# Optimization experiments

Hardware: AMD Instinct MI355X
Metric: run time of the kernel (lower is better)

Reference implementation:

```python
import jax, jax.numpy as jnp
import numpy as np

N = 256          # num agents
HID = 128        # hidden_dim
ACT = 5          # action_dim
NH = 4           # num_heads
D = HID + 16     # concat_hidden_dim = 144
E = D * NH       # mha embed dim = 576
HD = D           # per-head dim = E // NH = 144
OBS_RX, OBS_RY = 4, 2   # obs_r from fov_size=(9,5)
GRID = 40


def setup_inputs() -> dict:
    key = jax.random.key(0)
    ks = jax.random.split(key, 24)
    g = lambda k, shape, s: (jax.random.normal(k, shape, dtype=jnp.float32) * s)
    inp = {
        "hidden_state_n": g(ks[0], (N, HID), 1.0),
        "action_n": g(ks[1], (N, HID), 1.0),
        "state_n": jax.random.randint(ks[2], (N, 2), 0, GRID, dtype=jnp.int32),
        # obs encoder
        "W_enc": g(ks[3], (HID, 16), HID ** -0.5), "b_enc": jnp.zeros((16,), jnp.float32),
        # MHABlock outer projections
        "Wq": g(ks[4], (D, E), D ** -0.5), "bq": jnp.zeros((E,), jnp.float32),
        "Wk": g(ks[5], (D, E), D ** -0.5), "bk": jnp.zeros((E,), jnp.float32),
        "Wv": g(ks[6], (D, E), D ** -0.5), "bv": jnp.zeros((E,), jnp.float32),
        # nn.MultiheadAttention internal in/out projections
        "Wiq": g(ks[7], (E, E), E ** -0.5), "biq": jnp.zeros((E,), jnp.float32),
        "Wik": g(ks[8], (E, E), E ** -0.5), "bik": jnp.zeros((E,), jnp.float32),
        "Wiv": g(ks[9], (E, E), E ** -0.5), "biv": jnp.zeros((E,), jnp.float32),
        "Wo_proj": g(ks[10], (E, E), E ** -0.5), "bo_proj": jnp.zeros((E,), jnp.float32),
        "W_O": g(ks[11], (E, D), E ** -0.5),  # no bias
        # dueling decoders
        "W_val": g(ks[12], (D, 1), D ** -0.5), "b_val": jnp.zeros((1,), jnp.float32),
        "W_adv": g(ks[13], (D, ACT), D ** -0.5), "b_adv": jnp.zeros((ACT,), jnp.float32),
    }
    return inp


def reference(hidden_state_n, action_n, W_enc, b_enc, Wq, bq, Wk, bk, Wv, bv,
              Wiq, biq, Wik, bik, Wiv, biv, Wo_proj, bo_proj, W_O,
              W_val, b_val, W_adv, b_adv, state_n):
    n = hidden_state_n.shape[0]
    # observed_agents[i] = {j > i : |x_i-x_j|<=rx and |y_i-y_j|<=ry}
    pos = state_n.astype(jnp.int32)
    dx = jnp.abs(pos[:, None, 0] - pos[None, :, 0])
    dy = jnp.abs(pos[:, None, 1] - pos[None, :, 1])
    upper = jnp.arange(n)[None, :] > jnp.arange(n)[:, None]
    mask = (dx <= OBS_RX) & (dy <= OBS_RY) & upper            # [N,N], mask[i,j]: j observed by i

    # per-neighbor feature c_j = concat(obs_encoder(h_j), a_j)  -> [N, D]
    obs = hidden_state_n @ W_enc + b_enc                       # [N,16]
    C = jnp.concatenate([obs, action_n], axis=-1)              # [N,D]

    # MHABlock: outer Q/K/V projections then nn.MultiheadAttention
    q = (C @ Wq + bq) @ Wiq + biq                              # [N,E]
    k = (C @ Wk + bk) @ Wik + bik
    v = (C @ Wv + bv) @ Wiv + biv
    q2 = q.reshape(n, NH, HD)
    k2 = k.reshape(n, NH, HD)
    v2 = v.reshape(n, NH, HD)

    scale = 1.0 / np.sqrt(HD).astype(np.float32)
    S = jnp.einsum("jhd,khd->hjk", q2, k2) * scale             # [H,N,N] shared across agents

    pair = (mask[:, None, :, None] & mask[:, None, None, :])   # [N,1,Nq,Nk]
    logits = jnp.where(pair, S[None, :, :, :], -1e9)           # [N,H,N,N]
    m = jnp.max(logits, axis=-1, keepdims=True)
    p = jnp.exp(logits - m) * pair.astype(logits.dtype)
    attn = p / jnp.maximum(p.sum(axis=-1, keepdims=True), 1e-9)

    ctx = jnp.einsum("ihjk,khd->ijhd", attn, v2).reshape(n, n, E)  # [N,Nq,E]
    out = (ctx @ Wo_proj + bo_proj) @ W_O                          # [N,Nq,D]

    # sum over the (masked) neighbor/query axis -> per-agent h_i
    h = jnp.sum(out * mask[:, :, None].astype(out.dtype), axis=1)  # [N,D]

    V = h @ W_val + b_val                                          # [N,1]
    A = h @ W_adv + b_adv                                          # [N,ACT]
    Q = V + A - jnp.mean(A, axis=-1, keepdims=True)                # dueling Q
    return Q
```

## Files before the change

kernel.cpp:

```cpp
#include <hip/hip_runtime.h>

#define NAG 256
#define HID 128
#define ACT 5
#define NH 4
#define DD 144
#define EE 576
#define HDIM 144
#define CMAX 32

#define STEP4(acc, a) do { \
    acc.x += (a).x*wc0.x + (a).y*wc1.x + (a).z*wc2.x + (a).w*wc3.x; \
    acc.y += (a).x*wc0.y + (a).y*wc1.y + (a).z*wc2.y + (a).w*wc3.y; \
    acc.z += (a).x*wc0.z + (a).y*wc1.z + (a).z*wc2.z + (a).w*wc3.z; \
    acc.w += (a).x*wc0.w + (a).y*wc1.w + (a).z*wc2.w + (a).w*wc3.w; } while (0)

__device__ __forceinline__ void gemm8x64_sk(
    const float* __restrict__ A,
    const float* __restrict__ Wt,
    const float* __restrict__ bv,
    const float* __restrict__ rs,
    const float* __restrict__ rb,
    float* __restrict__ outp,
    int K, int lda, int ldw, int ldo, int nvalid,
    int tid, float* __restrict__ sm)
{
    const int lsa = K + 4;
    const int KF4 = K >> 2;
    for (int idx = tid; idx < 8 * KF4; idx += 256) {
        int r = idx / KF4, f = idx - r * KF4;
        *((float4*)&sm[r * lsa + f * 4]) =
            *(const float4*)(A + (size_t)r * lda + f * 4);
    }
    __syncthreads();
    const int wave = tid >> 6, lane = tid & 63;
    const int cg = lane & 15, rg = lane >> 4;
    const int co = cg * 4;
    const bool cok = (co + 4 <= nvalid);
    const int Kq = K >> 2;
    const int kbase = wave * Kq;
    const float* Wp = Wt + (size_t)kbase * ldw + (cok ? co : 0);
    float4 acc0 = {0.f, 0.f, 0.f, 0.f}, acc1 = {0.f, 0.f, 0.f, 0.f};
    float4 wc0, wc1, wc2, wc3;
    wc0 = *(const float4*)(Wp);
    wc1 = *(const float4*)(Wp + (size_t)ldw);
    wc2 = *(const float4*)(Wp + 2 * (size_t)ldw);
    wc3 = *(const float4*)(Wp + 3 * (size_t)ldw);
    const float* Asr = sm + (rg * 2) * lsa + kbase;
    const int NG = Kq >> 2;
    for (int g = 0; g < NG; ++g) {
        float4 nx0, nx1, nx2, nx3;
        if (g + 1 < NG) {
            const float* Wn = Wp + (size_t)(4 * (g + 1)) * ldw;
            nx0 = *(const float4*)(Wn);
            nx1 = *(const float4*)(Wn + (size_t)ldw);
            nx2 = *(const float4*)(Wn + 2 * (size_t)ldw);
            nx3 = *(const float4*)(Wn + 3 * (size_t)ldw);
        }
        float4 a0 = *((const float4*)(Asr + g * 4));
        float4 a1 = *((const float4*)(Asr + lsa + g * 4));
        STEP4(acc0, a0);
        STEP4(acc1, a1);
        wc0 = nx0; wc1 = nx1; wc2 = nx2; wc3 = nx3;
    }
    __syncthreads();
    float* red = sm;
    *((float4*)&red[wave * 512 + (rg * 2 + 0) * 64 + co]) = acc0;
    *((float4*)&red[wave * 512 + (rg * 2 + 1) * 64 + co]) = acc1;
    __syncthreads();
    #pragma unroll
    for (int qq = 0; qq < 2; ++qq) {
        int idx = tid + qq * 256;
        int r = idx >> 6, cl = idx & 63;
        if (cl < nvalid) {
            float s = red[idx] + red[512 + idx] + red[1024 + idx] + red[1536 + idx];
            float add = bv ? bv[cl] : 0.f;
            if (rs) add += rs[r] * rb[cl];
            outp[(size_t)r * ldo + cl] = s + add;
        }
    }
}

__global__ __launch_bounds__(256) void k_enc(
    const float* __restrict__ hidden, const float* __restrict__ action,
    const float* __restrict__ W_enc, const float* __restrict__ b_enc,
    float* __restrict__ C)
{
    __shared__ float Hs[8 * 132];
    __shared__ float We[2048];
    const int mb = blockIdx.x, tid = threadIdx.x;
    {
        int r = tid >> 5, kq = tid & 31;
        *((float4*)&Hs[r * 132 + kq * 4]) =
            *(const float4*)(hidden + (size_t)(mb * 8 + r) * HID + kq * 4);
        float4 a4 = *(const float4*)(action + (size_t)(mb * 8 + r) * HID + kq * 4);
        *((float4*)(C + (size_t)(mb * 8 + r) * DD + 16 + kq * 4)) = a4;
        *((float4*)&We[tid * 4])        = *(const float4*)(W_enc + tid * 4);
        *((float4*)&We[1024 + tid * 4]) = *(const float4*)(W_enc + 1024 + tid * 4);
    }
    __syncthreads();
    if (tid < 128) {
        int r = tid >> 4, o = tid & 15;
        float acc = 0.f;
        #pragma unroll 8
        for (int d = 0; d < HID; ++d) acc += Hs[r * 132 + d] * We[d * 16 + o];
        C[(size_t)(mb * 8 + r) * DD + o] = acc + b_enc[o];
    }
}

__global__ __launch_bounds__(256) void k_t3(
    const float* __restrict__ C,
    const float* __restrict__ Wq, const float* __restrict__ bq,
    const float* __restrict__ Wk, const float* __restrict__ bk,
    const float* __restrict__ Wv, const float* __restrict__ bv,
    float* __restrict__ Tq, float* __restrict__ Tk, float* __restrict__ Tv)
{
    __shared__ float sm[2048];
    const int z = blockIdx.z;
    const float* W = (z == 0) ? Wq : (z == 1) ? Wk : Wv;
    const float* b = (z == 0) ? bq : (z == 1) ? bk : bv;
    float*       T = (z == 0) ? Tq : (z == 1) ? Tk : Tv;
    const int rbase = blockIdx.x * 8, cb = blockIdx.y * 64;
    gemm8x64_sk(C + (size_t)rbase * DD, W + cb, b + cb, nullptr, nullptr,
                T + (size_t)rbase * EE + cb, DD, DD, EE, EE, 64,
                threadIdx.x, sm);
}

__global__ __launch_bounds__(256) void k_qkv3(
    const float* __restrict__ Tq, const float* __restrict__ Tk, const float* __restrict__ Tv,
    const float* __restrict__ Wiq, const float* __restrict__ biq,
    const float* __restrict__ Wik, const float* __restrict__ bik,
    const float* __restrict__ Wiv, const float* __restrict__ biv,
    float* __restrict__ q, float* __restrict__ kb, float* __restrict__ v)
{
    __shared__ float sm[8 * 580];
    const int z = blockIdx.z;
    const float* A = (z == 0) ? Tq  : (z == 1) ? Tk  : Tv;
    const float* W = (z == 0) ? Wiq : (z == 1) ? Wik : Wiv;
    const float* b = (z == 0) ? biq : (z == 1) ? bik : biv;
    float*       o = (z == 0) ? q   : (z == 1) ? kb  : v;
    const int rbase = blockIdx.x * 8, cb = blockIdx.y * 64;
    gemm8x64_sk(A + (size_t)rbase * EE, W + cb, b + cb, nullptr, nullptr,
                o + (size_t)rbase * EE + cb, EE, EE, EE, EE, 64,
                threadIdx.x, sm);
}

#define DOT4(a, b) ((a).x*(b).x + (a).y*(b).y + (a).z*(b).z + (a).w*(b).w)

__global__ __launch_bounds__(64) void k_score(
    const float* __restrict__ q, const float* __restrict__ kmat,
    float* __restrict__ S)
{
    __shared__ float Aq[8 * 148];
    __shared__ float Bk[64 * 148];
    const int tid = threadIdx.x;
    const int jb = blockIdx.x * 8, kbb = blockIdx.y * 64, h = blockIdx.z;
    const float* Ap = q    + (size_t)jb  * EE + h * HDIM;
    const float* Bp = kmat + (size_t)kbb * EE + h * HDIM;
    for (int idx = tid; idx < 8 * 36; idx += 64) {
        int r = idx / 36, f = idx - r * 36;
        *((float4*)&Aq[r * 148 + f * 4]) = *(const float4*)(Ap + (size_t)r * EE + f * 4);
    }
    for (int idx = tid; idx < 64 * 36; idx += 64) {
        int r = idx / 36, f = idx - r * 36;
        *((float4*)&Bk[r * 148 + f * 4]) = *(const float4*)(Bp + (size_t)r * EE + f * 4);
    }
    __syncthreads();
    const int cg = tid & 15, rg = tid >> 4;
    const int c0 = cg * 4;
    float4 acc0 = {0.f, 0.f, 0.f, 0.f}, acc1 = {0.f, 0.f, 0.f, 0.f};
    const float* A0 = Aq + (rg * 2) * 148;
    const float* A1 = A0 + 148;
    const float* B0 = Bk + (c0 + 0) * 148;
    const float* B1 = Bk + (c0 + 1) * 148;
    const float* B2 = Bk + (c0 + 2) * 148;
    const float* B3 = Bk + (c0 + 3) * 148;
    for (int g = 0; g < 36; ++g) {
        float4 a0 = *((const float4*)(A0 + g * 4));
        float4 a1 = *((const float4*)(A1 + g * 4));
        float4 b0 = *((const float4*)(B0 + g * 4));
        float4 b1 = *((const float4*)(B1 + g * 4));
        float4 b2 = *((const float4*)(B2 + g * 4));
        float4 b3 = *((const float4*)(B3 + g * 4));
        acc0.x += DOT4(a0, b0); acc0.y += DOT4(a0, b1);
        acc0.z += DOT4(a0, b2); acc0.w += DOT4(a0, b3);
        acc1.x += DOT4(a1, b0); acc1.y += DOT4(a1, b1);
        acc1.z += DOT4(a1, b2); acc1.w += DOT4(a1, b3);
    }
    const float SC = 1.0f / 12.0f;
    float* Sp = S + ((size_t)(h * NAG + jb + rg * 2)) * NAG + kbb + c0;
    float4 o0 = { acc0.x * SC, acc0.y * SC, acc0.z * SC, acc0.w * SC };
    float4 o1 = { acc1.x * SC, acc1.y * SC, acc1.z * SC, acc1.w * SC };
    *(float4*)Sp = o0;
    *(float4*)(Sp + NAG) = o1;
}

__global__ __launch_bounds__(256) void k_agent(
    const int* __restrict__ state, const float* __restrict__ S,
    const float* __restrict__ v,
    float* __restrict__ ctxsum, float* __restrict__ cnt)
{
    __shared__ int lst[NAG];
    __shared__ int cnt_s;
    __shared__ float w4[NH][NAG];
    __shared__ float Sl[NH][CMAX][CMAX + 1];
    const int i = blockIdx.x, tid = threadIdx.x;
    if (tid == 0) cnt_s = 0;
    __syncthreads();
    {
        int xi = state[2 * i], yi = state[2 * i + 1];
        int xj = state[2 * tid], yj = state[2 * tid + 1];
        int dx = xi - xj; if (dx < 0) dx = -dx;
        int dy = yi - yj; if (dy < 0) dy = -dy;
        if (tid > i && dx <= 4 && dy <= 2) {
            int p = atomicAdd(&cnt_s, 1);
            lst[p] = tid;
        }
    }
    __syncthreads();
    const int c = cnt_s;
    if (tid == 0) cnt[i] = (float)c;
    if (c == 0) {
        for (int e = tid; e < EE; e += 256) ctxsum[(size_t)i * EE + e] = 0.f;
        return;
    }
    if (c <= CMAX) {
        for (int idx = tid; idx < NH * c * c; idx += 256) {
            int h = idx / (c * c), rem = idx - h * c * c;
            int jj = rem / c, kk = rem - jj * c;
            Sl[h][jj][kk] = S[((size_t)(h * NAG + lst[jj])) * NAG + lst[kk]];
        }
        __syncthreads();
        if (tid < NH * c) {
            int h = tid / c, jj = tid - h * c;
            float m = -1e30f;
            for (int kk = 0; kk < c; ++kk) m = fmaxf(m, Sl[h][jj][kk]);
            float zz = 0.f;
            for (int kk = 0; kk < c; ++kk) {
                float e = __expf(Sl[h][jj][kk] - m);
                Sl[h][jj][kk] = e;
                zz += e;
            }
            float inv = 1.f / fmaxf(zz, 1e-9f);
            for (int kk = 0; kk < c; ++kk) Sl[h][jj][kk] *= inv;
        }
        __syncthreads();
        if (tid < NH * c) {
            int h = tid / c, kk = tid - h * c;
            float s = 0.f;
            for (int jj = 0; jj < c; ++jj) s += Sl[h][jj][kk];
            w4[h][kk] = s;
        }
        __syncthreads();
    } else {
        for (int idx = tid; idx < NH * c; idx += 256) w4[idx / c][idx % c] = 0.f;
        __syncthreads();
        for (int t = tid; t < NH * c; t += 256) {
            int h = t / c, jj = t - h * c;
            const float* Srow = S + ((size_t)(h * NAG + lst[jj])) * NAG;
            float m = -1e30f;
            for (int kk = 0; kk < c; ++kk) m = fmaxf(m, Srow[lst[kk]]);
            float zz = 0.f;
            for (int kk = 0; kk < c; ++kk) zz += __expf(Srow[lst[kk]] - m);
            float inv = 1.f / fmaxf(zz, 1e-9f);
            for (int kk = 0; kk < c; ++kk)
                atomicAdd(&w4[h][kk], __expf(Srow[lst[kk]] - m) * inv);
        }
        __syncthreads();
    }
    for (int e = tid; e < EE; e += 256) {
        int h = e / HDIM;
        float a0 = 0.f, a1 = 0.f;
        int t = 0;
        for (; t + 1 < c; t += 2) {
            a0 += w4[h][t] * v[(size_t)lst[t] * EE + e];
            a1 += w4[h][t + 1] * v[(size_t)lst[t + 1] * EE + e];
        }
        if (t < c) a0 += w4[h][t] * v[(size_t)lst[t] * EE + e];
        ctxsum[(size_t)i * EE + e] = a0 + a1;
    }
}

__global__ __launch_bounds__(256) void k_g(
    const float* __restrict__ ctx, const float* __restrict__ Wo,
    const float* __restrict__ bo, const float* __restrict__ cnt,
    float* __restrict__ g)
{
    __shared__ float sm[8 * 580];
    const int rbase = blockIdx.x * 8, cb = blockIdx.y * 64;
    gemm8x64_sk(ctx + (size_t)rbase * EE, Wo + cb, nullptr, cnt + rbase, bo + cb,
                g + (size_t)rbase * EE + cb, EE, EE, EE, EE, 64,
                threadIdx.x, sm);
}

__global__ __launch_bounds__(256) void k_h(
    const float* __restrict__ g, const float* __restrict__ W_O,
    float* __restrict__ hbuf)
{
    __shared__ float sm[8 * 580];
    const int rbase = blockIdx.x * 8, cb = blockIdx.y * 64;
    const int nv = DD - cb;
    gemm8x64_sk(g + (size_t)rbase * EE, W_O + cb, nullptr, nullptr, nullptr,
                hbuf + (size_t)rbase * DD + cb, EE, EE, DD, DD,
                (nv < 64) ? nv : 64, threadIdx.x, sm);
}

__global__ __launch_bounds__(256) void k_head(
    const float* __restrict__ hbuf,
    const float* __restrict__ W_val, const float* __restrict__ b_val,
    const float* __restrict__ W_adv, const float* __restrict__ b_adv,
    float* __restrict__ out)
{
    const int ag = blockIdx.x * 4 + (threadIdx.x >> 6);
    const int lane = threadIdx.x & 63;
    const float* hp = hbuf + (size_t)ag * DD;
    float h0 = hp[lane], h1 = hp[lane + 64];
    float h2 = (lane < 16) ? hp[lane + 128] : 0.f;
    float red[6];
    for (int o = 0; o < 6; ++o) {
        float p;
        if (o < 5) {
            p = h0 * W_adv[lane * ACT + o] + h1 * W_adv[(lane + 64) * ACT + o];
            if (lane < 16) p += h2 * W_adv[(lane + 128) * ACT + o];
        } else {
            p = h0 * W_val[lane] + h1 * W_val[lane + 64];
            if (lane < 16) p += h2 * W_val[lane + 128];
        }
        for (int off = 32; off; off >>= 1) p += __shfl_xor(p, off);
        red[o] = p;
    }
    if (lane == 0) {
        float a[ACT], mean = 0.f;
        for (int o = 0; o < ACT; ++o) { a[o] = red[o] + b_adv[o]; mean += a[o]; }
        mean *= (1.0f / ACT);
        float V = red[5] + b_val[0];
        for (int o = 0; o < ACT; ++o) out[ag * ACT + o] = V + a[o] - mean;
    }
}

extern "C" void kernel_launch(void* const* d_in, const int* in_sizes, int n_in,
                              void* d_out, int out_size, void* d_ws, size_t ws_size,
                              hipStream_t stream)
{
    const float* hidden = (const float*)d_in[0];
    const float* action = (const float*)d_in[1];
    const int*   state  = (const int*)d_in[2];
    const float* W_enc  = (const float*)d_in[3];
    const float* b_enc  = (const float*)d_in[4];
    const float* Wq     = (const float*)d_in[5];
    const float* bq     = (const float*)d_in[6];
    const float* Wk     = (const float*)d_in[7];
    const float* bk     = (const float*)d_in[8];
    const float* Wv     = (const float*)d_in[9];
    const float* bv     = (const float*)d_in[10];
    const float* Wiq    = (const float*)d_in[11];
    const float* biq    = (const float*)d_in[12];
    const float* Wik    = (const float*)d_in[13];
    const float* bik    = (const float*)d_in[14];
    const float* Wiv    = (const float*)d_in[15];
    const float* biv    = (const float*)d_in[16];
    const float* Wo     = (const float*)d_in[17];
    const float* bo     = (const float*)d_in[18];
    const float* W_O    = (const float*)d_in[19];
    const float* W_val  = (const float*)d_in[20];
    const float* b_val  = (const float*)d_in[21];
    const float* W_adv  = (const float*)d_in[22];
    const float* b_adv  = (const float*)d_in[23];
    float* outp = (float*)d_out;

    float* ws = (float*)d_ws;
    float* C    = ws;
    float* Tq   = C    + NAG * DD;
    float* Tk   = Tq   + NAG * EE;
    float* Tv   = Tk   + NAG * EE;
    float* q    = Tv   + NAG * EE;
    float* kb   = q    + NAG * EE;
    float* v    = kb   + NAG * EE;
    float* S    = v    + NAG * EE;
    float* ctx  = S    + NH * NAG * NAG;
    float* g    = ctx  + NAG * EE;
    float* hbuf = g    + NAG * EE;
    float* cnt  = hbuf + NAG * DD;

    k_enc<<<32, 256, 0, stream>>>(hidden, action, W_enc, b_enc, C);
    k_t3<<<dim3(32, 9, 3), 256, 0, stream>>>(C, Wq, bq, Wk, bk, Wv, bv, Tq, Tk, Tv);
    k_qkv3<<<dim3(32, 9, 3), 256, 0, stream>>>(Tq, Tk, Tv, Wiq, biq, Wik, bik,
                                               Wiv, biv, q, kb, v);
    k_score<<<dim3(32, 4, 4), 64, 0, stream>>>(q, kb, S);
    k_agent<<<NAG, 256, 0, stream>>>(state, S, v, ctx, cnt);
    k_g<<<dim3(32, 9), 256, 0, stream>>>(ctx, Wo, bo, cnt, g);
    k_h<<<dim3(32, 3), 256, 0, stream>>>(g, W_O, hbuf);
    k_head<<<64, 256, 0, stream>>>(hbuf, W_val, b_val, W_adv, b_adv, outp);
}
```

Measured before the change: 191.6 us.

## Fuse encoder into first projection and W_O projection into dueling head

The obs-encoder kernel is merged into the first Q/K/V projection kernel, so each block recomputes its 8-row slice of C in shared memory instead of reading it from a global buffer. The W_O projection and the dueling value/advantage head are merged into one kernel that keeps h in shared memory. Together this removes two kernel launches and the global round-trips for C and hbuf. In exchange the encoder work is repeated 27 times per row block, and the fused head kernel runs only 32 blocks that loop serially over three column tiles.

After: 200.4 us. 1.05x slower.

```diff
diff --git a/kernel.cpp b/kernel.cpp
--- a/kernel.cpp
+++ b/kernel.cpp
@@ -15,24 +15,16 @@
     acc.z += (a).x*wc0.z + (a).y*wc1.z + (a).z*wc2.z + (a).w*wc3.z; \
     acc.w += (a).x*wc0.w + (a).y*wc1.w + (a).z*wc2.w + (a).w*wc3.w; } while (0)
 
-__device__ __forceinline__ void gemm8x64_sk(
-    const float* __restrict__ A,
+__device__ __forceinline__ void gemm8x64_core(
+    const float* __restrict__ Asm, int lsa,
     const float* __restrict__ Wt,
     const float* __restrict__ bv,
     const float* __restrict__ rs,
-    const float* __restrict__ rb,
+    const float* __restrict__ rbias,
     float* __restrict__ outp,
-    int K, int lda, int ldw, int ldo, int nvalid,
-    int tid, float* __restrict__ sm)
-{
-    const int lsa = K + 4;
-    const int KF4 = K >> 2;
-    for (int idx = tid; idx < 8 * KF4; idx += 256) {
-        int r = idx / KF4, f = idx - r * KF4;
-        *((float4*)&sm[r * lsa + f * 4]) =
-            *(const float4*)(A + (size_t)r * lda + f * 4);
-    }
-    __syncthreads();
+    int K, int ldw, int ldo, int nvalid,
+    int tid, float* __restrict__ red)
+{
     const int wave = tid >> 6, lane = tid & 63;
     const int cg = lane & 15, rg = lane >> 4;
     const int co = cg * 4;
@@ -46,7 +38,7 @@
     wc1 = *(const float4*)(Wp + (size_t)ldw);
     wc2 = *(const float4*)(Wp + 2 * (size_t)ldw);
     wc3 = *(const float4*)(Wp + 3 * (size_t)ldw);
-    const float* Asr = sm + (rg * 2) * lsa + kbase;
+    const float* Asr = Asm + (rg * 2) * lsa + kbase;
     const int NG = Kq >> 2;
     for (int g = 0; g < NG; ++g) {
         float4 nx0, nx1, nx2, nx3;
@@ -64,7 +56,6 @@
         wc0 = nx0; wc1 = nx1; wc2 = nx2; wc3 = nx3;
     }
     __syncthreads();
-    float* red = sm;
     *((float4*)&red[wave * 512 + (rg * 2 + 0) * 64 + co]) = acc0;
     *((float4*)&red[wave * 512 + (rg * 2 + 1) * 64 + co]) = acc1;
     __syncthreads();
@@ -75,26 +66,54 @@
         if (cl < nvalid) {
             float s = red[idx] + red[512 + idx] + red[1024 + idx] + red[1536 + idx];
             float add = bv ? bv[cl] : 0.f;
-            if (rs) add += rs[r] * rb[cl];
+            if (rs) add += rs[r] * rbias[cl];
             outp[(size_t)r * ldo + cl] = s + add;
         }
     }
 }
 
-__global__ __launch_bounds__(256) void k_enc(
+__device__ __forceinline__ void gemm8x64_sk(
+    const float* __restrict__ A, const float* __restrict__ Wt,
+    const float* __restrict__ bv, const float* __restrict__ rs,
+    const float* __restrict__ rbias, float* __restrict__ outp,
+    int K, int lda, int ldw, int ldo, int nvalid,
+    int tid, float* __restrict__ sm)
+{
+    const int lsa = K + 4;
+    const int KF4 = K >> 2;
+    for (int idx = tid; idx < 8 * KF4; idx += 256) {
+        int r = idx / KF4, f = idx - r * KF4;
+        *((float4*)&sm[r * lsa + f * 4]) =
+            *(const float4*)(A + (size_t)r * lda + f * 4);
+    }
+    __syncthreads();
+    gemm8x64_core(sm, lsa, Wt, bv, rs, rbias, outp, K, ldw, ldo, nvalid,
+                  tid, sm );
+}
+
+__global__ __launch_bounds__(256) void k_t3e(
     const float* __restrict__ hidden, const float* __restrict__ action,
     const float* __restrict__ W_enc, const float* __restrict__ b_enc,
-    float* __restrict__ C)
-{
-    __shared__ float Hs[8 * 132];
-    __shared__ float We[2048];
-    const int mb = blockIdx.x, tid = threadIdx.x;
+    const float* __restrict__ Wq, const float* __restrict__ bq,
+    const float* __restrict__ Wk, const float* __restrict__ bk,
+    const float* __restrict__ Wv, const float* __restrict__ bv,
+    float* __restrict__ Tq, float* __restrict__ Tk, float* __restrict__ Tv)
+{
+    __shared__ float sm[4288];
+    float* C8 = sm;
+    float* Hs = sm + 1184;
+    float* We = sm + 2240;
+    const int tid = threadIdx.x;
+    const int row0 = blockIdx.x * 8, cb = blockIdx.y * 64, z = blockIdx.z;
+    const float* Wz = (z == 0) ? Wq : (z == 1) ? Wk : Wv;
+    const float* bz = (z == 0) ? bq : (z == 1) ? bk : bv;
+    float*       T  = (z == 0) ? Tq : (z == 1) ? Tk : Tv;
     {
         int r = tid >> 5, kq = tid & 31;
         *((float4*)&Hs[r * 132 + kq * 4]) =
-            *(const float4*)(hidden + (size_t)(mb * 8 + r) * HID + kq * 4);
-        float4 a4 = *(const float4*)(action + (size_t)(mb * 8 + r) * HID + kq * 4);
-        *((float4*)(C + (size_t)(mb * 8 + r) * DD + 16 + kq * 4)) = a4;
+            *(const float4*)(hidden + (size_t)(row0 + r) * HID + kq * 4);
+        float4 a4 = *(const float4*)(action + (size_t)(row0 + r) * HID + kq * 4);
+        *((float4*)&C8[r * 148 + 16 + kq * 4]) = a4;
         *((float4*)&We[tid * 4])        = *(const float4*)(W_enc + tid * 4);
         *((float4*)&We[1024 + tid * 4]) = *(const float4*)(W_enc + 1024 + tid * 4);
     }
@@ -104,26 +123,12 @@
         float acc = 0.f;
         #pragma unroll 8
         for (int d = 0; d < HID; ++d) acc += Hs[r * 132 + d] * We[d * 16 + o];
-        C[(size_t)(mb * 8 + r) * DD + o] = acc + b_enc[o];
-    }
-}
-
-__global__ __launch_bounds__(256) void k_t3(
-    const float* __restrict__ C,
-    const float* __restrict__ Wq, const float* __restrict__ bq,
-    const float* __restrict__ Wk, const float* __restrict__ bk,
-    const float* __restrict__ Wv, const float* __restrict__ bv,
-    float* __restrict__ Tq, float* __restrict__ Tk, float* __restrict__ Tv)
-{
-    __shared__ float sm[2048];
-    const int z = blockIdx.z;
-    const float* W = (z == 0) ? Wq : (z == 1) ? Wk : Wv;
-    const float* b = (z == 0) ? bq : (z == 1) ? bk : bv;
-    float*       T = (z == 0) ? Tq : (z == 1) ? Tk : Tv;
-    const int rbase = blockIdx.x * 8, cb = blockIdx.y * 64;
-    gemm8x64_sk(C + (size_t)rbase * DD, W + cb, b + cb, nullptr, nullptr,
-                T + (size_t)rbase * EE + cb, DD, DD, EE, EE, 64,
-                threadIdx.x, sm);
+        C8[r * 148 + o] = acc + b_enc[o];
+    }
+    __syncthreads();
+    gemm8x64_core(C8, 148, Wz + cb, bz + cb, nullptr, nullptr,
+                  T + (size_t)row0 * EE + cb, DD, EE, EE, 64,
+                  tid, sm + 1184 );
 }
 
 __global__ __launch_bounds__(256) void k_qkv3(
@@ -293,48 +298,57 @@
                 threadIdx.x, sm);
 }
 
-__global__ __launch_bounds__(256) void k_h(
+__global__ __launch_bounds__(256) void k_hh(
     const float* __restrict__ g, const float* __restrict__ W_O,
-    float* __restrict__ hbuf)
-{
-    __shared__ float sm[8 * 580];
-    const int rbase = blockIdx.x * 8, cb = blockIdx.y * 64;
-    const int nv = DD - cb;
-    gemm8x64_sk(g + (size_t)rbase * EE, W_O + cb, nullptr, nullptr, nullptr,
-                hbuf + (size_t)rbase * DD + cb, EE, EE, DD, DD,
-                (nv < 64) ? nv : 64, threadIdx.x, sm);
-}
-
-__global__ __launch_bounds__(256) void k_head(
-    const float* __restrict__ hbuf,
     const float* __restrict__ W_val, const float* __restrict__ b_val,
     const float* __restrict__ W_adv, const float* __restrict__ b_adv,
     float* __restrict__ out)
 {
-    const int ag = blockIdx.x * 4 + (threadIdx.x >> 6);
-    const int lane = threadIdx.x & 63;
-    const float* hp = hbuf + (size_t)ag * DD;
-    float h0 = hp[lane], h1 = hp[lane + 64];
-    float h2 = (lane < 16) ? hp[lane + 128] : 0.f;
-    float red[6];
-    for (int o = 0; o < 6; ++o) {
-        float p;
-        if (o < 5) {
-            p = h0 * W_adv[lane * ACT + o] + h1 * W_adv[(lane + 64) * ACT + o];
-            if (lane < 16) p += h2 * W_adv[(lane + 128) * ACT + o];
-        } else {
-            p = h0 * W_val[lane] + h1 * W_val[lane + 64];
-            if (lane < 16) p += h2 * W_val[lane + 128];
-        }
-        for (int off = 32; off; off >>= 1) p += __shfl_xor(p, off);
-        red[o] = p;
-    }
-    if (lane == 0) {
-        float a[ACT], mean = 0.f;
-        for (int o = 0; o < ACT; ++o) { a[o] = red[o] + b_adv[o]; mean += a[o]; }
-        mean *= (1.0f / ACT);
-        float V = red[5] + b_val[0];
-        for (int o = 0; o < ACT; ++o) out[ag * ACT + o] = V + a[o] - mean;
+    __shared__ float sm[7872];
+    float* gsm = sm;
+    float* red = sm + 4640;
+    float* hsm = sm + 6688;
+    const int tid = threadIdx.x;
+    const int a0 = blockIdx.x * 8;
+    for (int idx = tid; idx < 8 * 144; idx += 256) {
+        int r = idx / 144, f = idx - r * 144;
+        *((float4*)&gsm[r * 580 + f * 4]) =
+            *(const float4*)(g + (size_t)(a0 + r) * EE + f * 4);
+    }
+    __syncthreads();
+    #pragma unroll
+    for (int cb = 0; cb < 144; cb += 64) {
+        const int nv = (144 - cb < 64) ? (144 - cb) : 64;
+        gemm8x64_core(gsm, 580, W_O + cb, nullptr, nullptr, nullptr,
+                      hsm + cb, EE, DD, 148, nv, tid, red);
+        __syncthreads();
+    }
+    const int wave = tid >> 6, lane = tid & 63;
+    for (int s = 0; s < 2; ++s) {
+        const int ag = wave * 2 + s;
+        const float* hp = hsm + ag * 148;
+        float h0 = hp[lane], h1 = hp[lane + 64];
+        float h2 = (lane < 16) ? hp[lane + 128] : 0.f;
+        float red6[6];
+        for (int o = 0; o < 6; ++o) {
+            float p;
+            if (o < 5) {
+                p = h0 * W_adv[lane * ACT + o] + h1 * W_adv[(lane + 64) * ACT + o];
+                if (lane < 16) p += h2 * W_adv[(lane + 128) * ACT + o];
+            } else {
+                p = h0 * W_val[lane] + h1 * W_val[lane + 64];
+                if (lane < 16) p += h2 * W_val[lane + 128];
+            }
+            for (int off = 32; off; off >>= 1) p += __shfl_xor(p, off);
+            red6[o] = p;
+        }
+        if (lane == 0) {
+            float a[ACT], mean = 0.f;
+            for (int o = 0; o < ACT; ++o) { a[o] = red6[o] + b_adv[o]; mean += a[o]; }
+            mean *= (1.0f / ACT);
+            float V = red6[5] + b_val[0];
+            for (int o = 0; o < ACT; ++o) out[(a0 + ag) * ACT + o] = V + a[o] - mean;
+        }
     }
 }
 
@@ -369,8 +383,7 @@
     float* outp = (float*)d_out;
 
     float* ws = (float*)d_ws;
-    float* C    = ws;
-    float* Tq   = C    + NAG * DD;
+    float* Tq   = ws;
     float* Tk   = Tq   + NAG * EE;
     float* Tv   = Tk   + NAG * EE;
     float* q    = Tv   + NAG * EE;
@@ -379,16 +392,14 @@
     float* S    = v    + NAG * EE;
     float* ctx  = S    + NH * NAG * NAG;
     float* g    = ctx  + NAG * EE;
-    float* hbuf = g    + NAG * EE;
-    float* cnt  = hbuf + NAG * DD;
-
-    k_enc<<<32, 256, 0, stream>>>(hidden, action, W_enc, b_enc, C);
-    k_t3<<<dim3(32, 9, 3), 256, 0, stream>>>(C, Wq, bq, Wk, bk, Wv, bv, Tq, Tk, Tv);
+    float* cnt  = g    + NAG * EE;
+
+    k_t3e<<<dim3(32, 9, 3), 256, 0, stream>>>(hidden, action, W_enc, b_enc,
+                                              Wq, bq, Wk, bk, Wv, bv, Tq, Tk, Tv);
     k_qkv3<<<dim3(32, 9, 3), 256, 0, stream>>>(Tq, Tk, Tv, Wiq, biq, Wik, bik,
                                                Wiv, biv, q, kb, v);
     k_score<<<dim3(32, 4, 4), 64, 0, stream>>>(q, kb, S);
     k_agent<<<NAG, 256, 0, stream>>>(state, S, v, ctx, cnt);
     k_g<<<dim3(32, 9), 256, 0, stream>>>(ctx, Wo, bo, cnt, g);
-    k_h<<<dim3(32, 3), 256, 0, stream>>>(g, W_O, hbuf);
-    k_head<<<64, 256, 0, stream>>>(hbuf, W_val, b_val, W_adv, b_adv, outp);
-}
+    k_hh<<<32, 256, 0, stream>>>(g, W_O, W_val, b_val, W_adv, b_adv, outp);
+}
```
